# Kernel optimization log

Hardware: AMD Instinct MI355X
Metric: run time of the kernel (lower is better)

## Reference

```python
import jax, jax.numpy as jnp
import numpy as np

N = 50000
E = 800000
NUM_GRAPHS = 64
D_IN = 261
D_SAGE = 64
D_LIN = 32
N_SAGE_REST = 6
N_LIN_REST = 3
EPS = 1e-5


def _layernorm(x, g, b):
    mu = jnp.mean(x, axis=-1, keepdims=True)
    var = jnp.mean((x - mu) ** 2, axis=-1, keepdims=True)
    return (x - mu) * jax.lax.rsqrt(var + EPS) * g + b


def _sage_block(x, Wl, bl, Wr, g, b, src, dst, inv_deg, residual):
    # mean aggregation of neighbor (source) features onto targets
    msum = jax.ops.segment_sum(x[src], dst, num_segments=N)  # [N, d]
    mean = msum * inv_deg  # [N, d]
    f = mean @ Wl + bl + x @ Wr  # lin_l(aggr) + lin_r(x); lin_r has no bias
    f = jax.nn.gelu(f, approximate=False)
    f = _layernorm(f, g, b)
    if residual:
        f = f + x
    return f


def _lin_block(x, W, b, g, beta, residual):
    f = jax.nn.gelu(x @ W + b, approximate=False)
    f = _layernorm(f, g, beta)
    if residual:
        f = f + x
    return f


def setup_inputs() -> dict:
    key = jax.random.key(0)
    ks = jax.random.split(key, 24)
    x = jax.random.normal(ks[0], (N, D_IN), dtype=jnp.float32)
    edge_index = jax.random.randint(ks[1], (2, E), 0, N, dtype=jnp.int64)
    batch = jnp.sort(jax.random.randint(ks[2], (N,), 0, NUM_GRAPHS, dtype=jnp.int64))

    def glorot(k, shape):
        fan_in = shape[0]
        return jax.random.normal(k, shape, dtype=jnp.float32) / np.sqrt(fan_in)

    inp = {
        "x": x, "edge_index": edge_index, "batch": batch,
        # first SAGE block (261 -> 64, no residual)
        "Wl0": glorot(ks[3], (D_IN, D_SAGE)), "bl0": jnp.zeros((D_SAGE,), jnp.float32),
        "Wr0": glorot(ks[4], (D_IN, D_SAGE)),
        "g0": jnp.ones((D_SAGE,), jnp.float32), "beta0": jnp.zeros((D_SAGE,), jnp.float32),
        # 6 residual SAGE blocks (64 -> 64), stacked
        "Wl": glorot(ks[5], (N_SAGE_REST, D_SAGE, D_SAGE)),
        "bl": jnp.zeros((N_SAGE_REST, D_SAGE), jnp.float32),
        "Wr": glorot(ks[6], (N_SAGE_REST, D_SAGE, D_SAGE)),
        "g": jnp.ones((N_SAGE_REST, D_SAGE), jnp.float32),
        "beta": jnp.zeros((N_SAGE_REST, D_SAGE), jnp.float32),
        # MLP: first LinearBlock 64 -> 32 (no residual)
        "M0": glorot(ks[7], (D_SAGE, D_LIN)), "mb0": jnp.zeros((D_LIN,), jnp.float32),
        "mg0": jnp.ones((D_LIN,), jnp.float32), "mbeta0": jnp.zeros((D_LIN,), jnp.float32),
        # 3 residual LinearBlocks 32 -> 32, stacked
        "M": glorot(ks[8], (N_LIN_REST, D_LIN, D_LIN)),
        "mb": jnp.zeros((N_LIN_REST, D_LIN), jnp.float32),
        "mg": jnp.ones((N_LIN_REST, D_LIN), jnp.float32),
        "mbeta": jnp.zeros((N_LIN_REST, D_LIN), jnp.float32),
        # final Linear 32 -> 1
        "Wf": glorot(ks[9], (D_LIN, 1)), "bf": jnp.zeros((1,), jnp.float32),
    }
    return inp


def reference(x, edge_index, batch, Wl0, bl0, Wr0, g0, beta0, Wl, bl, Wr, g, beta,
              M0, mb0, mg0, mbeta0, M, mb, mg, mbeta, Wf, bf):
    src, dst = edge_index[0], edge_index[1]
    deg = jax.ops.segment_sum(jnp.ones((E,), x.dtype), dst, num_segments=N)
    inv_deg = (1.0 / jnp.maximum(deg, 1.0))[:, None]  # [N,1]

    h = _sage_block(x, Wl0, bl0, Wr0, g0, beta0, src, dst, inv_deg, residual=False)
    for i in range(N_SAGE_REST):
        h = _sage_block(h, Wl[i], bl[i], Wr[i], g[i], beta[i], src, dst, inv_deg, residual=True)

    pooled = jax.ops.segment_sum(h, batch, num_segments=NUM_GRAPHS)  # [G, 64]

    m = _lin_block(pooled, M0, mb0, mg0, mbeta0, residual=False)
    for i in range(N_LIN_REST):
        m = _lin_block(m, M[i], mb[i], mg[i], mbeta[i], residual=True)
    return m @ Wf + bf  # [G, 1]
```

## Files before the change

kernel.cpp:

```cpp
#include <hip/hip_runtime.h>
#include <hip/hip_bf16.h>
#include <math.h>

#define N_NODES 50000
#define N_EDGES 800000
#define NUM_GRAPHS 64
#define NPAD 50048
#define KPAD0 288
#define PSPLIT 16
#define MAXDEG 64

#define GEMM0_GRID (NPAD / 64)
#define LAYER_GRID (NPAD / 32)
#define ZERO_GRID  ((N_NODES + 255) / 256)
#define PREPW_TOT  (128 * KPAD0 + 6 * 128 * 64)
#define PREPW_GRID ((PREPW_TOT + 255) / 256)

#define SLICES 8
#define NPS 6250
#define SCHUNK 2048
#define SCHUNKS ((N_EDGES + SCHUNK - 1) / SCHUNK)
#define SCAT_GRID (SCHUNKS * SLICES)

typedef __attribute__((ext_vector_type(8))) short short8;
typedef __attribute__((ext_vector_type(4))) float f32x4;

__device__ __forceinline__ float gelu_f(float v) {
    return 0.5f * v * (1.0f + erff(v * 0.70710678118654752440f));
}

__device__ __forceinline__ float half_sum32(float v) {
    v += __shfl_xor(v, 1); v += __shfl_xor(v, 2); v += __shfl_xor(v, 4);
    v += __shfl_xor(v, 8); v += __shfl_xor(v, 16);
    return v;
}

__device__ __forceinline__ float group_sum8(float v) {
    v += __shfl_xor(v, 1); v += __shfl_xor(v, 2); v += __shfl_xor(v, 4);
    return v;
}

__device__ __forceinline__ unsigned short f2bf(float f) {
    unsigned int u = __float_as_uint(f);
    unsigned int r = (u + 0x7fffu + ((u >> 16) & 1u)) >> 16;
    return (unsigned short)r;
}

__device__ __forceinline__ float bf_lo(unsigned int u) {
    return __uint_as_float(u << 16);
}
__device__ __forceinline__ float bf_hi(unsigned int u) {
    return __uint_as_float(u & 0xffff0000u);
}


__global__ void k_prep(int* __restrict__ deg,
                       const float* __restrict__ Wl0, const float* __restrict__ Wr0,
                       const float* __restrict__ Wl, const float* __restrict__ Wr,
                       unsigned short* __restrict__ Bt0, unsigned short* __restrict__ BtR) {
    const int blk = blockIdx.x, tid = threadIdx.x;
    if (blk < ZERO_GRID) {
        int i = blk * 256 + tid;
        if (i < N_NODES) deg[i] = 0;
        return;
    }
    int idx = (blk - ZERO_GRID) * 256 + tid;
    const int n0 = 128 * KPAD0;
    if (idx < n0) {
        int j = idx / KPAD0, k = idx - j * KPAD0;
        float v = 0.0f;
        if (k < 261) v = (j < 64) ? Wl0[k * 64 + j] : Wr0[k * 64 + (j - 64)];
        Bt0[idx] = f2bf(v);
    } else if (idx < PREPW_TOT) {
        int r = idx - n0;
        int l = r >> 13;
        int rr = r & 8191;
        int j = rr >> 6, k = rr & 63;
        float v = (j < 64) ? Wl[l * 4096 + k * 64 + j] : Wr[l * 4096 + k * 64 + (j - 64)];
        BtR[r] = f2bf(v);
    }
}


__global__ __launch_bounds__(256) void k_gemm0(
        const float* __restrict__ X, const unsigned short* __restrict__ Bt0,
        unsigned short* __restrict__ U, float* __restrict__ V) {
    __shared__ __align__(16) unsigned short sA[64 * 32];
    __shared__ __align__(16) unsigned short sB[128 * 32];
    const int tid = threadIdx.x;
    const int lane = tid & 63, wid = tid >> 6;
    const int l16 = lane & 15, quad = lane >> 4;
    const int m0 = blockIdx.x * 64;
    f32x4 acc[8];
    #pragma unroll
    for (int j = 0; j < 8; ++j) { acc[j][0] = 0.f; acc[j][1] = 0.f; acc[j][2] = 0.f; acc[j][3] = 0.f; }
    const int arow = tid >> 2, apart = (tid & 3) << 3;
    const int node = m0 + arow;
    const int rowok = (node < N_NODES);
    for (int kc = 0; kc < KPAD0; kc += 32) {
        if (kc) __syncthreads();
        short8 av;
        #pragma unroll
        for (int j = 0; j < 8; ++j) {
            int kk = kc + apart + j;
            float val = (rowok && kk < 261) ? X[(size_t)node * 261 + kk] : 0.0f;
            av[j] = (short)f2bf(val);
        }
        *(short8*)&sA[arow * 32 + apart] = av;
        #pragma unroll
        for (int q = 0; q < 2; ++q) {
            int flat = q * 256 + tid;
            int br = flat >> 2, bp = (flat & 3) << 3;
            *(int4*)&sB[br * 32 + bp] = *(const int4*)&Bt0[(size_t)br * KPAD0 + kc + bp];
        }
        __syncthreads();
        short8 af = *(const short8*)&sA[(wid * 16 + l16) * 32 + quad * 8];
        #pragma unroll
        for (int j = 0; j < 8; ++j) {
            short8 bf = *(const short8*)&sB[(j * 16 + l16) * 32 + quad * 8];
            acc[j] = __builtin_amdgcn_mfma_f32_16x16x32_bf16(af, bf, acc[j], 0, 0, 0);
        }
    }
    const int rbase = m0 + wid * 16 + quad * 4;
    #pragma unroll
    for (int j = 0; j < 4; ++j)
        #pragma unroll
        for (int r = 0; r < 4; ++r)
            U[(size_t)(rbase + r) * 64 + j * 16 + l16] = f2bf(acc[j][r]);
    #pragma unroll
    for (int j = 4; j < 8; ++j)
        #pragma unroll
        for (int r = 0; r < 4; ++r)
            V[(size_t)(rbase + r) * 64 + (j - 4) * 16 + l16] = acc[j][r];
}


__global__ __launch_bounds__(256) void k_scat(
        const int* __restrict__ src, const int* __restrict__ dst,
        int* __restrict__ deg, unsigned short* __restrict__ col64) {
    const int s = blockIdx.x & (SLICES - 1);
    const int c = blockIdx.x >> 3;
    const int base = c * SCHUNK;
    const int lim = min(base + SCHUNK, N_EDGES);
    for (int i = base + (int)threadIdx.x; i < lim; i += 256) {
        int d = dst[i];
        int sv = src[i];
        if (d / NPS == s) {
            int pos = atomicAdd(&deg[d], 1);
            if (pos < MAXDEG) col64[(d << 6) + pos] = (unsigned short)sv;
        }
    }
}


__global__ __launch_bounds__(256, 4) void k_layer(
        const unsigned short* __restrict__ U_in, const float* __restrict__ V_in,
        unsigned short* __restrict__ h,
        float* __restrict__ hf_out,
        const int* __restrict__ deg, const unsigned short* __restrict__ col64,
        const float* __restrict__ bias, const float* __restrict__ gam,
        const float* __restrict__ bet,
        const unsigned short* __restrict__ Bt_next,
        unsigned short* __restrict__ U_out, float* __restrict__ V_out,
        int residual, int have_gemm) {
    __shared__ __align__(16) unsigned short sA[2 * 32 * 32];
    __shared__ __align__(16) unsigned short sB[128 * 32];
    const int tid = threadIdx.x;
    const int lane = tid & 63, wid = tid >> 6;
    const int sub = lane >> 3, hl = lane & 7;
    const int base = lane & 56;
    const int m0 = blockIdx.x * 32;
    const uint4* __restrict__ Up = (const uint4*)U_in;

    const int nl = wid * 8 + sub;
    const int node = m0 + nl;
    const bool valid = (node < N_NODES);
    const int nd = valid ? node : 0;
    const int dg = valid ? deg[nd] : 0;
    const int cnt = min(dg, MAXDEG);
    uint4 cv = make_uint4(0u, 0u, 0u, 0u);
    if (valid) cv = *(const uint4*)&col64[((size_t)nd << 6) + hl * 8];
    float s0 = 0.f, s1 = 0.f, s2 = 0.f, s3 = 0.f, s4 = 0.f, s5 = 0.f, s6 = 0.f, s7 = 0.f;
    for (int b = 0; b * 8 < cnt; b += 2) {
        #pragma unroll
        for (int hh = 0; hh < 2; ++hh) {
            const int sl = base + b + hh;
            unsigned int p0 = (unsigned int)__shfl((int)cv.x, sl);
            unsigned int p1 = (unsigned int)__shfl((int)cv.y, sl);
            unsigned int p2 = (unsigned int)__shfl((int)cv.z, sl);
            unsigned int p3 = (unsigned int)__shfl((int)cv.w, sl);
            const int eb = (b + hh) * 8;
            int c[8];
            c[0] = (int)(p0 & 0xffffu); c[1] = (int)(p0 >> 16);
            c[2] = (int)(p1 & 0xffffu); c[3] = (int)(p1 >> 16);
            c[4] = (int)(p2 & 0xffffu); c[5] = (int)(p2 >> 16);
            c[6] = (int)(p3 & 0xffffu); c[7] = (int)(p3 >> 16);
            #pragma unroll
            for (int i = 0; i < 8; ++i) {
                uint4 u = (eb + i < cnt) ? Up[(size_t)c[i] * 8 + hl] : make_uint4(0u, 0u, 0u, 0u);
                s0 += bf_lo(u.x); s1 += bf_hi(u.x);
                s2 += bf_lo(u.y); s3 += bf_hi(u.y);
                s4 += bf_lo(u.z); s5 += bf_hi(u.z);
                s6 += bf_lo(u.w); s7 += bf_hi(u.w);
            }
        }
    }
    const float id = 1.0f / fmaxf((float)dg, 1.0f);
    const float4 b0 = *(const float4*)&bias[8 * hl];
    const float4 b1 = *(const float4*)&bias[8 * hl + 4];
    float4 v0 = make_float4(0.f, 0.f, 0.f, 0.f), v1 = v0;
    if (valid) {
        v0 = *(const float4*)&V_in[(size_t)nd * 64 + 8 * hl];
        v1 = *(const float4*)&V_in[(size_t)nd * 64 + 8 * hl + 4];
    }
    float f0 = gelu_f(s0 * id + b0.x + v0.x);
    float f1 = gelu_f(s1 * id + b0.y + v0.y);
    float f2 = gelu_f(s2 * id + b0.z + v0.z);
    float f3 = gelu_f(s3 * id + b0.w + v0.w);
    float f4 = gelu_f(s4 * id + b1.x + v1.x);
    float f5 = gelu_f(s5 * id + b1.y + v1.y);
    float f6 = gelu_f(s6 * id + b1.z + v1.z);
    float f7 = gelu_f(s7 * id + b1.w + v1.w);
    float mu = group_sum8(((f0 + f1) + (f2 + f3)) + ((f4 + f5) + (f6 + f7))) * 0.015625f;
    float d0 = f0 - mu, d1 = f1 - mu, d2 = f2 - mu, d3 = f3 - mu;
    float d4 = f4 - mu, d5 = f5 - mu, d6 = f6 - mu, d7 = f7 - mu;
    float var = group_sum8(((d0 * d0 + d1 * d1) + (d2 * d2 + d3 * d3)) +
                           ((d4 * d4 + d5 * d5) + (d6 * d6 + d7 * d7))) * 0.015625f;
    float rs = rsqrtf(var + 1e-5f);
    const float4 g0v = *(const float4*)&gam[8 * hl];
    const float4 g1v = *(const float4*)&gam[8 * hl + 4];
    const float4 e0v = *(const float4*)&bet[8 * hl];
    const float4 e1v = *(const float4*)&bet[8 * hl + 4];
    f0 = d0 * rs * g0v.x + e0v.x;
    f1 = d1 * rs * g0v.y + e0v.y;
    f2 = d2 * rs * g0v.z + e0v.z;
    f3 = d3 * rs * g0v.w + e0v.w;
    f4 = d4 * rs * g1v.x + e1v.x;
    f5 = d5 * rs * g1v.y + e1v.y;
    f6 = d6 * rs * g1v.z + e1v.z;
    f7 = d7 * rs * g1v.w + e1v.w;
    if (residual && valid) {
        uint4 hu = ((const uint4*)h)[(size_t)nd * 8 + hl];
        f0 += bf_lo(hu.x); f1 += bf_hi(hu.x);
        f2 += bf_lo(hu.y); f3 += bf_hi(hu.y);
        f4 += bf_lo(hu.z); f5 += bf_hi(hu.z);
        f6 += bf_lo(hu.w); f7 += bf_hi(hu.w);
    }
    uint4 outw;
    outw.x = (unsigned int)f2bf(f0) | ((unsigned int)f2bf(f1) << 16);
    outw.y = (unsigned int)f2bf(f2) | ((unsigned int)f2bf(f3) << 16);
    outw.z = (unsigned int)f2bf(f4) | ((unsigned int)f2bf(f5) << 16);
    outw.w = (unsigned int)f2bf(f6) | ((unsigned int)f2bf(f7) << 16);
    if (valid) {
        ((uint4*)h)[(size_t)nd * 8 + hl] = outw;
        if (hf_out) {
            *(float4*)&hf_out[(size_t)nd * 64 + 8 * hl] = make_float4(f0, f1, f2, f3);
            *(float4*)&hf_out[(size_t)nd * 64 + 8 * hl + 4] = make_float4(f4, f5, f6, f7);
        }
    }
    *(uint4*)&sA[(((hl >> 2) * 32 + nl) << 5) + (hl & 3) * 8] = outw;

    if (!have_gemm) return;
    __syncthreads();

    const int l16 = lane & 15, quad = lane >> 4;
    const int wrow = wid & 1, colh = wid >> 1;
    f32x4 acc[4];
    #pragma unroll
    for (int j = 0; j < 4; ++j) { acc[j][0] = 0.f; acc[j][1] = 0.f; acc[j][2] = 0.f; acc[j][3] = 0.f; }
    for (int kc = 0; kc < 64; kc += 32) {
        if (kc) __syncthreads();
        #pragma unroll
        for (int q = 0; q < 2; ++q) {
            int flat = q * 256 + tid;
            int br = flat >> 2, bp = (flat & 3) << 3;
            *(int4*)&sB[br * 32 + bp] = *(const int4*)&Bt_next[(size_t)br * 64 + kc + bp];
        }
        __syncthreads();
        short8 af = *(const short8*)&sA[(((kc >> 5) * 32 + wrow * 16 + l16) << 5) + quad * 8];
        #pragma unroll
        for (int j = 0; j < 4; ++j) {
            short8 bf = *(const short8*)&sB[(colh * 64 + j * 16 + l16) * 32 + quad * 8];
            acc[j] = __builtin_amdgcn_mfma_f32_16x16x32_bf16(af, bf, acc[j], 0, 0, 0);
        }
    }
    const int rbase = m0 + wrow * 16 + quad * 4;
    if (colh == 0) {
        #pragma unroll
        for (int j = 0; j < 4; ++j)
            #pragma unroll
            for (int r = 0; r < 4; ++r)
                U_out[(size_t)(rbase + r) * 64 + j * 16 + l16] = f2bf(acc[j][r]);
    } else {
        #pragma unroll
        for (int j = 0; j < 4; ++j)
            #pragma unroll
            for (int r = 0; r < 4; ++r)
                V_out[(size_t)(rbase + r) * 64 + j * 16 + l16] = acc[j][r];
    }
}


__global__ __launch_bounds__(256) void k_pool1(const float* __restrict__ h, const int* __restrict__ batch,
                                               float* __restrict__ partial, int n) {
    __shared__ float sred[4][64];
    const int g = blockIdx.x / PSPLIT;
    const int s = blockIdx.x - g * PSPLIT;
    const int lane = threadIdx.x & 63, wid = threadIdx.x >> 6;
    int lo = 0, hi = n;
    while (lo < hi) { int mid = (lo + hi) >> 1; if (batch[mid] < g) lo = mid + 1; else hi = mid; }
    const int start = lo;
    lo = 0; hi = n;
    while (lo < hi) { int mid = (lo + hi) >> 1; if (batch[mid] < g + 1) lo = mid + 1; else hi = mid; }
    const int end = lo;
    const int len = end - start;
    const int chunk = (len + PSPLIT - 1) / PSPLIT;
    const int a = start + s * chunk;
    const int b = min(a + chunk, end);
    float sum = 0.0f;
    for (int node = a + wid; node < b; node += 4) sum += h[(size_t)node * 64 + lane];
    sred[wid][lane] = sum;
    __syncthreads();
    if (wid == 0)
        partial[(size_t)blockIdx.x * 64 + lane] = sred[0][lane] + sred[1][lane] + sred[2][lane] + sred[3][lane];
}


__global__ __launch_bounds__(1024) void k_head(const float* __restrict__ partial,
                                               const float* __restrict__ M0, const float* __restrict__ mb0,
                                               const float* __restrict__ mg0, const float* __restrict__ mbeta0,
                                               const float* __restrict__ M, const float* __restrict__ mb,
                                               const float* __restrict__ mg, const float* __restrict__ mbeta,
                                               const float* __restrict__ Wf, const float* __restrict__ bf,
                                               float* __restrict__ out) {
    __shared__ float sP[64 * 64];
    __shared__ float sA[64 * 33];
    __shared__ float sB[64 * 33];
    const int tx = threadIdx.x, ty = threadIdx.y;
    const int tid = ty * 32 + tx;
    for (int i = tid; i < 64 * 64; i += 1024) {
        int g = i >> 6, f = i & 63;
        float s = 0.0f;
        #pragma unroll
        for (int s2 = 0; s2 < PSPLIT; ++s2) s += partial[(size_t)(g * PSPLIT + s2) * 64 + f];
        sP[i] = s;
    }
    __syncthreads();
    #pragma unroll
    for (int rr = 0; rr < 2; ++rr) {
        int r = ty + rr * 32;
        float a = mb0[tx];
        for (int k = 0; k < 64; ++k) a += sP[r * 64 + k] * M0[k * 32 + tx];
        a = gelu_f(a);
        float mu = half_sum32(a) * (1.0f / 32.0f);
        float d = a - mu;
        float var = half_sum32(d * d) * (1.0f / 32.0f);
        a = d * rsqrtf(var + 1e-5f) * mg0[tx] + mbeta0[tx];
        sA[r * 33 + tx] = a;
    }
    __syncthreads();
    float* cur = sA;
    float* nxt = sB;
    for (int L = 0; L < 3; ++L) {
        const float* Mi = M + L * 32 * 32;
        const float* mbi = mb + L * 32;
        const float* mgi = mg + L * 32;
        const float* mbetai = mbeta + L * 32;
        #pragma unroll
        for (int rr = 0; rr < 2; ++rr) {
            int r = ty + rr * 32;
            float a = mbi[tx];
            for (int k = 0; k < 32; ++k) a += cur[r * 33 + k] * Mi[k * 32 + tx];
            a = gelu_f(a);
            float mu = half_sum32(a) * (1.0f / 32.0f);
            float d = a - mu;
            float var = half_sum32(d * d) * (1.0f / 32.0f);
            a = d * rsqrtf(var + 1e-5f) * mgi[tx] + mbetai[tx] + cur[r * 33 + tx];
            nxt[r * 33 + tx] = a;
        }
        __syncthreads();
        float* t = cur; cur = nxt; nxt = t;
    }
    #pragma unroll
    for (int rr = 0; rr < 2; ++rr) {
        int r = ty + rr * 32;
        float p = cur[r * 33 + tx] * Wf[tx];
        p = half_sum32(p);
        if (tx == 0) out[r] = p + bf[0];
    }
}


extern "C" void kernel_launch(void* const* d_in, const int* in_sizes, int n_in,
                              void* d_out, int out_size, void* d_ws, size_t ws_size,
                              hipStream_t stream) {
    const int N = N_NODES;
    const int E = N_EDGES;

    const float* x    = (const float*)d_in[0];
    const int* eidx   = (const int*)d_in[1];
    const int* batch  = (const int*)d_in[2];
    const float* Wl0  = (const float*)d_in[3];
    const float* bl0  = (const float*)d_in[4];
    const float* Wr0  = (const float*)d_in[5];
    const float* g0   = (const float*)d_in[6];
    const float* bet0 = (const float*)d_in[7];
    const float* Wl   = (const float*)d_in[8];
    const float* bl   = (const float*)d_in[9];
    const float* Wr   = (const float*)d_in[10];
    const float* gR   = (const float*)d_in[11];
    const float* betR = (const float*)d_in[12];
    const float* M0   = (const float*)d_in[13];
    const float* mb0  = (const float*)d_in[14];
    const float* mg0  = (const float*)d_in[15];
    const float* mbe0 = (const float*)d_in[16];
    const float* M    = (const float*)d_in[17];
    const float* mb   = (const float*)d_in[18];
    const float* mg   = (const float*)d_in[19];
    const float* mbe  = (const float*)d_in[20];
    const float* Wf   = (const float*)d_in[21];
    const float* bf   = (const float*)d_in[22];

    const int* src = eidx;
    const int* dst = eidx + E;

    char* p = (char*)d_ws;
    auto alloc = [&](size_t bytes) -> void* {
        void* q = (void*)p;
        p += (bytes + 255) & ~(size_t)255;
        return q;
    };
    int*   deg    = (int*)alloc((size_t)N * 4);
    unsigned short* col64 = (unsigned short*)alloc((size_t)N * MAXDEG * 2);
    unsigned short* Bt0 = (unsigned short*)alloc((size_t)128 * KPAD0 * 2);
    unsigned short* BtR = (unsigned short*)alloc((size_t)6 * 128 * 64 * 2);
    unsigned short* Ua  = (unsigned short*)alloc((size_t)NPAD * 64 * 2);
    unsigned short* Ub  = (unsigned short*)alloc((size_t)NPAD * 64 * 2);
    float* Va   = (float*)alloc((size_t)NPAD * 64 * 4);
    float* Vb   = (float*)alloc((size_t)NPAD * 64 * 4);
    unsigned short* hbuf = (unsigned short*)alloc((size_t)NPAD * 64 * 2);
    float* partial = (float*)alloc((size_t)NUM_GRAPHS * PSPLIT * 64 * 4);

    k_prep<<<ZERO_GRID + PREPW_GRID, 256, 0, stream>>>(deg, Wl0, Wr0, Wl, Wr, Bt0, BtR);

    k_scat<<<SCAT_GRID, 256, 0, stream>>>(src, dst, deg, col64);

    k_gemm0<<<GEMM0_GRID, 256, 0, stream>>>(x, Bt0, Ua, Va);

    unsigned short* Uin = Ua;  float* Vin = Va;
    unsigned short* Uout = Ub; float* Vout = Vb;
    for (int i = 0; i < 7; ++i) {
        const float* bias = (i == 0) ? bl0  : bl  + (size_t)(i - 1) * 64;
        const float* gam  = (i == 0) ? g0   : gR  + (size_t)(i - 1) * 64;
        const float* bet  = (i == 0) ? bet0 : betR + (size_t)(i - 1) * 64;
        const int have_gemm = (i < 6);
        float* hf = (i == 6) ? Vout : nullptr;
        k_layer<<<LAYER_GRID, 256, 0, stream>>>(
            Uin, Vin, hbuf, hf, deg, col64, bias, gam, bet,
            have_gemm ? (BtR + (size_t)i * 128 * 64) : BtR,
            Uout, Vout, (i > 0) ? 1 : 0, have_gemm);
        unsigned short* tu = Uin; Uin = Uout; Uout = tu;
        float* tv = Vin; Vin = Vout; Vout = tv;
    }
    float* hf_final = Vin;

    k_pool1<<<NUM_GRAPHS * PSPLIT, 256, 0, stream>>>(hf_final, batch, partial, N);
    k_head<<<1, dim3(32, 32), 0, stream>>>(partial, M0, mb0, mg0, mbe0, M, mb, mg, mbe, Wf, bf, (float*)d_out);
}
```

Before: 375.4 us.

## Pre-convert X to padded bf16 alongside edge scatter; drop LDS staging in GEMMs

Adds a pass, merged into the scatter kernel's grid, that converts the fp32 input features into a padded bf16 buffer so the first GEMM can load MFMA fragments straight from global memory with no shared-memory staging or barriers. The layer kernel likewise reads its next-layer weight fragments directly from global or cache instead of staging them in LDS, and its occupancy launch bound is removed. This trades an extra write and read of about 29 MB of bf16 features, plus uncoalesced fragment loads, for fewer synchronisations and overlap of the conversion with the atomic-bound scatter.

```diff
diff --git a/kernel.cpp b/kernel.cpp
--- a/kernel.cpp
+++ b/kernel.cpp
@@ -21,6 +21,7 @@
 #define SCHUNK 2048
 #define SCHUNKS ((N_EDGES + SCHUNK - 1) / SCHUNK)
 #define SCAT_GRID (SCHUNKS * SLICES)
+#define CONV_GRID (NPAD * (KPAD0 / 8) / 256)
 
 typedef __attribute__((ext_vector_type(8))) short short8;
 typedef __attribute__((ext_vector_type(4))) float f32x4;
@@ -82,11 +83,49 @@
 }
 
 
+__global__ __launch_bounds__(256) void k_scat(
+        const int* __restrict__ src, const int* __restrict__ dst,
+        int* __restrict__ deg, unsigned short* __restrict__ col64,
+        const float* __restrict__ X, unsigned short* __restrict__ Xbf) {
+    const int blk = blockIdx.x;
+    const int tid = threadIdx.x;
+    if (blk < SCAT_GRID) {
+        const int s = blk & (SLICES - 1);
+        const int c = blk >> 3;
+        const int base = c * SCHUNK;
+        const int lim = min(base + SCHUNK, N_EDGES);
+        for (int i = base + tid; i < lim; i += 256) {
+            int d = dst[i];
+            int sv = src[i];
+            if (d / NPS == s) {
+                int pos = atomicAdd(&deg[d], 1);
+                if (pos < MAXDEG) col64[(d << 6) + pos] = (unsigned short)sv;
+            }
+        }
+    } else {
+        int t = (blk - SCAT_GRID) * 256 + tid;
+        int node = t / (KPAD0 / 8);
+        int k8 = (t - node * (KPAD0 / 8)) * 8;
+        short8 v8;
+        if (node < N_NODES) {
+            #pragma unroll
+            for (int j = 0; j < 8; ++j) {
+                int k = k8 + j;
+                float val = (k < 261) ? X[(size_t)node * 261 + k] : 0.0f;
+                v8[j] = (short)f2bf(val);
+            }
+        } else {
+            #pragma unroll
+            for (int j = 0; j < 8; ++j) v8[j] = 0;
+        }
+        *(short8*)&Xbf[(size_t)node * KPAD0 + k8] = v8;
+    }
+}
+
+
 __global__ __launch_bounds__(256) void k_gemm0(
-        const float* __restrict__ X, const unsigned short* __restrict__ Bt0,
+        const unsigned short* __restrict__ Xbf, const unsigned short* __restrict__ Bt0,
         unsigned short* __restrict__ U, float* __restrict__ V) {
-    __shared__ __align__(16) unsigned short sA[64 * 32];
-    __shared__ __align__(16) unsigned short sB[128 * 32];
     const int tid = threadIdx.x;
     const int lane = tid & 63, wid = tid >> 6;
     const int l16 = lane & 15, quad = lane >> 4;
@@ -94,31 +133,14 @@
     f32x4 acc[8];
     #pragma unroll
     for (int j = 0; j < 8; ++j) { acc[j][0] = 0.f; acc[j][1] = 0.f; acc[j][2] = 0.f; acc[j][3] = 0.f; }
-    const int arow = tid >> 2, apart = (tid & 3) << 3;
-    const int node = m0 + arow;
-    const int rowok = (node < N_NODES);
+    const unsigned short* xr = Xbf + (size_t)(m0 + wid * 16 + l16) * KPAD0 + quad * 8;
+    const unsigned short* br = Bt0 + (size_t)l16 * KPAD0 + quad * 8;
     for (int kc = 0; kc < KPAD0; kc += 32) {
-        if (kc) __syncthreads();
-        short8 av;
+        short8 af = *(const short8*)(xr + kc);
         #pragma unroll
         for (int j = 0; j < 8; ++j) {
-            int kk = kc + apart + j;
-            float val = (rowok && kk < 261) ? X[(size_t)node * 261 + kk] : 0.0f;
-            av[j] = (short)f2bf(val);
-        }
-        *(short8*)&sA[arow * 32 + apart] = av;
-        #pragma unroll
-        for (int q = 0; q < 2; ++q) {
-            int flat = q * 256 + tid;
-            int br = flat >> 2, bp = (flat & 3) << 3;
-            *(int4*)&sB[br * 32 + bp] = *(const int4*)&Bt0[(size_t)br * KPAD0 + kc + bp];
-        }
-        __syncthreads();
-        short8 af = *(const short8*)&sA[(wid * 16 + l16) * 32 + quad * 8];
-        #pragma unroll
-        for (int j = 0; j < 8; ++j) {
-            short8 bf = *(const short8*)&sB[(j * 16 + l16) * 32 + quad * 8];
-            acc[j] = __builtin_amdgcn_mfma_f32_16x16x32_bf16(af, bf, acc[j], 0, 0, 0);
+            short8 bfv = *(const short8*)(br + (size_t)j * 16 * KPAD0 + kc);
+            acc[j] = __builtin_amdgcn_mfma_f32_16x16x32_bf16(af, bfv, acc[j], 0, 0, 0);
         }
     }
     const int rbase = m0 + wid * 16 + quad * 4;
@@ -135,25 +157,7 @@
 }
 
 
-__global__ __launch_bounds__(256) void k_scat(
-        const int* __restrict__ src, const int* __restrict__ dst,
-        int* __restrict__ deg, unsigned short* __restrict__ col64) {
-    const int s = blockIdx.x & (SLICES - 1);
-    const int c = blockIdx.x >> 3;
-    const int base = c * SCHUNK;
-    const int lim = min(base + SCHUNK, N_EDGES);
-    for (int i = base + (int)threadIdx.x; i < lim; i += 256) {
-        int d = dst[i];
-        int sv = src[i];
-        if (d / NPS == s) {
-            int pos = atomicAdd(&deg[d], 1);
-            if (pos < MAXDEG) col64[(d << 6) + pos] = (unsigned short)sv;
-        }
-    }
-}
-
-
-__global__ __launch_bounds__(256, 4) void k_layer(
+__global__ __launch_bounds__(256) void k_layer(
         const unsigned short* __restrict__ U_in, const float* __restrict__ V_in,
         unsigned short* __restrict__ h,
         float* __restrict__ hf_out,
@@ -164,7 +168,6 @@
         unsigned short* __restrict__ U_out, float* __restrict__ V_out,
         int residual, int have_gemm) {
     __shared__ __align__(16) unsigned short sA[2 * 32 * 32];
-    __shared__ __align__(16) unsigned short sB[128 * 32];
     const int tid = threadIdx.x;
     const int lane = tid & 63, wid = tid >> 6;
     const int sub = lane >> 3, hl = lane & 7;
@@ -268,20 +271,13 @@
     f32x4 acc[4];
     #pragma unroll
     for (int j = 0; j < 4; ++j) { acc[j][0] = 0.f; acc[j][1] = 0.f; acc[j][2] = 0.f; acc[j][3] = 0.f; }
+    #pragma unroll
     for (int kc = 0; kc < 64; kc += 32) {
-        if (kc) __syncthreads();
-        #pragma unroll
-        for (int q = 0; q < 2; ++q) {
-            int flat = q * 256 + tid;
-            int br = flat >> 2, bp = (flat & 3) << 3;
-            *(int4*)&sB[br * 32 + bp] = *(const int4*)&Bt_next[(size_t)br * 64 + kc + bp];
-        }
-        __syncthreads();
         short8 af = *(const short8*)&sA[(((kc >> 5) * 32 + wrow * 16 + l16) << 5) + quad * 8];
         #pragma unroll
         for (int j = 0; j < 4; ++j) {
-            short8 bf = *(const short8*)&sB[(colh * 64 + j * 16 + l16) * 32 + quad * 8];
-            acc[j] = __builtin_amdgcn_mfma_f32_16x16x32_bf16(af, bf, acc[j], 0, 0, 0);
+            short8 bfv = *(const short8*)&Bt_next[(size_t)(colh * 64 + j * 16 + l16) * 64 + kc + quad * 8];
+            acc[j] = __builtin_amdgcn_mfma_f32_16x16x32_bf16(af, bfv, acc[j], 0, 0, 0);
         }
     }
     const int rbase = m0 + wrow * 16 + quad * 4;
@@ -434,6 +430,7 @@
     unsigned short* col64 = (unsigned short*)alloc((size_t)N * MAXDEG * 2);
     unsigned short* Bt0 = (unsigned short*)alloc((size_t)128 * KPAD0 * 2);
     unsigned short* BtR = (unsigned short*)alloc((size_t)6 * 128 * 64 * 2);
+    unsigned short* Xbf = (unsigned short*)alloc((size_t)NPAD * KPAD0 * 2);
     unsigned short* Ua  = (unsigned short*)alloc((size_t)NPAD * 64 * 2);
     unsigned short* Ub  = (unsigned short*)alloc((size_t)NPAD * 64 * 2);
     float* Va   = (float*)alloc((size_t)NPAD * 64 * 4);
@@ -443,9 +440,9 @@
 
     k_prep<<<ZERO_GRID + PREPW_GRID, 256, 0, stream>>>(deg, Wl0, Wr0, Wl, Wr, Bt0, BtR);
 
-    k_scat<<<SCAT_GRID, 256, 0, stream>>>(src, dst, deg, col64);
-
-    k_gemm0<<<GEMM0_GRID, 256, 0, stream>>>(x, Bt0, Ua, Va);
+    k_scat<<<SCAT_GRID + CONV_GRID, 256, 0, stream>>>(src, dst, deg, col64, x, Xbf);
+
+    k_gemm0<<<GEMM0_GRID, 256, 0, stream>>>(Xbf, Bt0, Ua, Va);
 
     unsigned short* Uin = Ua;  float* Vin = Va;
     unsigned short* Uout = Ub; float* Vout = Vb;
```

New measurement: 402.2 us. +7.2%, slower.
